# Kernel tuning notes

Hardware: AMD Instinct MI355X
Metric: run time of the kernel (lower is better)

The kernel has to match this reference:

```python
import jax, jax.numpy as jnp
import numpy as np

B, NM, MB, D = 16, 64, 64, 1024
NH, NKV, MEM = 16, 8, 64
HD = D // NH            # 64
S = MB + MEM            # per-step attention length
EPS = 1e-6

def precompute_freqs_cis(dim, end, theta=10000.0):
    freqs = 1.0 / (theta ** (jnp.arange(0, dim, 2)[: dim // 2].astype(jnp.float32) / dim))
    t = jnp.arange(end, dtype=jnp.float32)
    return jnp.exp(1j * jnp.outer(t, freqs))  # [end, dim//2] complex64

def apply_rope(x, fcis):
    # x: [s, h, d], fcis: [s, d//2] complex
    xc = x.reshape(x.shape[0], x.shape[1], HD // 2, 2)
    xc = jax.lax.complex(xc[..., 0], xc[..., 1]) * fcis[:, None, :]
    return jnp.stack([jnp.real(xc), jnp.imag(xc)], axis=-1).reshape(x.shape)

def layer_norm(x, scale, bias):
    m = x.mean(-1, keepdims=True)
    v = x.var(-1, keepdims=True)
    return (x - m) * jax.lax.rsqrt(v + EPS) * scale + bias

def setup_inputs() -> dict:
    key = jax.random.key(0)
    ks = jax.random.split(key, 8)
    s = 1.0 / np.sqrt(D)
    return {
        'hidden_states': jax.random.normal(ks[0], (B, NM, MB, D), jnp.float32),
        'mask': jax.random.bernoulli(ks[1], 0.9, (B, NM)),
        'mem_state': jax.random.normal(ks[2], (MEM, D), jnp.float32) * s,
        'wq': jax.random.normal(ks[3], (D, D), jnp.float32) * s,
        'wk': jax.random.normal(ks[4], (D, NKV * HD), jnp.float32) * s,
        'wv': jax.random.normal(ks[5], (D, NKV * HD), jnp.float32) * s,
        'wo': jax.random.normal(ks[6], (D, D), jnp.float32) * s,
        'pre_scale': jnp.ones((D,), jnp.float32),
        'pre_bias': jnp.zeros((D,), jnp.float32),
        'post_scale': jnp.ones((D,), jnp.float32),
        'post_bias': jnp.zeros((D,), jnp.float32),
    }

def reference(hidden_states, mask, mem_state, wq, wk, wv, wo, pre_scale, pre_bias, post_scale, post_bias):
    fcis = precompute_freqs_cis(HD, S)  # constant RoPE buffer, first S positions used
    rep = NH // NKV
    scale = 1.0 / np.sqrt(HD)

    def step(mem, inp):
        x_mb, m = inp  # x_mb: [MB, D], m: scalar bool
        h = layer_norm(jnp.concatenate([x_mb, mem], axis=0), pre_scale, pre_bias)  # [S, D]
        q = (h @ wq).reshape(S, NH, HD)
        k = (h @ wk).reshape(S, NKV, HD)
        v = (h @ wv).reshape(S, NKV, HD)
        q = apply_rope(q, fcis)
        k = apply_rope(k, fcis)
        k = jnp.repeat(k, rep, axis=1)  # GQA: expand kv heads
        v = jnp.repeat(v, rep, axis=1)
        qb, kb, vb = q.astype(jnp.bfloat16), k.astype(jnp.bfloat16), v.astype(jnp.bfloat16)
        logits = jnp.einsum('qhd,khd->hqk', qb, kb).astype(jnp.float32) * scale
        att = jax.nn.softmax(logits, axis=-1).astype(jnp.bfloat16)
        enc = jnp.einsum('hqk,khd->qhd', att, vb).reshape(S, D).astype(jnp.float32)
        out = enc[-MEM:] @ wo  # only memory-slot queries feed the update
        new_mem = layer_norm(out + mem, post_scale, post_bias)
        new_mem = jnp.where(m, new_mem, mem)  # lax.cond branch as select
        return new_mem, None

    def per_batch(x, m):
        final, _ = jax.lax.scan(step, mem_state, (x, m))
        return final

    return jax.vmap(per_batch)(hidden_states, mask)  # [B, MEM, D]
```

## Files before the change

kernel.cpp:

```cpp
#include <hip/hip_runtime.h>


typedef __attribute__((ext_vector_type(8))) _Float16 f16x8;
typedef __attribute__((ext_vector_type(4))) _Float16 f16x4;
typedef __attribute__((ext_vector_type(8))) short    s16x8;
typedef __attribute__((ext_vector_type(4))) float    f32x4;

#define NB   16
#define NMs  64
#define MBs  64
#define Dm   1024
#define NHh  16
#define NKVh 8
#define HDd  64
#define MEMm 64
#define Sq   128

__device__ __align__(16) _Float16      g_W1t[2048 * 1024];
__device__ __align__(16) _Float16      g_Wot[1024 * 1024];
__device__ __align__(16) float         g_rc[128 * 32];
__device__ __align__(16) float         g_rs[128 * 32];
__device__                unsigned char g_mask[NB * NMs];
__device__ __align__(16) _Float16      g_hx[(size_t)NB * NMs * MBs * Dm];
__device__ __align__(16) _Float16      g_hmem[NB * MEMm * Dm];
__device__ __align__(16) float         g_memA[NB * MEMm * Dm];
__device__ __align__(16) float         g_memB[NB * MEMm * Dm];
__device__ __align__(16) unsigned short g_qb[NB * NHh * 64 * 64];
__device__ __align__(16) unsigned short g_kb[NB * NKVh * 128 * 64];
__device__ __align__(16) unsigned short g_vt[NB * NKVh * 64 * 128];
__device__ __align__(16) _Float16      g_enc[NB * 64 * Dm];
__device__ __align__(16) float         g_outp[NB * 64 * Dm];

__device__ __forceinline__ unsigned short f2bf(float x) {
    union { float f; unsigned u; } v; v.f = x;
    unsigned u = v.u;
    return (unsigned short)((u + 0x7fffu + ((u >> 16) & 1u)) >> 16);
}
__device__ __forceinline__ float bf2f(unsigned short h) {
    union { unsigned u; float f; } v; v.u = ((unsigned)h) << 16; return v.f;
}

__device__ __forceinline__ void block_stats(float s, float ss, float eps,
                                            float* mean, float* rstd) {
    for (int off = 32; off > 0; off >>= 1) {
        s  += __shfl_down(s, off);
        ss += __shfl_down(ss, off);
    }
    __shared__ float red[8];
    int wid = threadIdx.x >> 6, lane = threadIdx.x & 63;
    __syncthreads();
    if (lane == 0) { red[wid] = s; red[4 + wid] = ss; }
    __syncthreads();
    float ts  = red[0] + red[1] + red[2] + red[3];
    float tss = red[4] + red[5] + red[6] + red[7];
    float m   = ts * (1.0f / 1024.0f);
    float var = tss * (1.0f / 1024.0f) - m * m;
    *mean = m;
    *rstd = rsqrtf(var + eps);
}

__global__ void k_transpose(const float* __restrict__ in, int ncols, int dsel) {
    _Float16* out = (dsel == 0) ? g_W1t
                  : (dsel == 1) ? (g_W1t + 1024 * 1024)
                  : (dsel == 2) ? (g_W1t + 1536 * 1024)
                                : g_Wot;
    __shared__ float tile[64][65];
    int bk = blockIdx.x, bn = blockIdx.y;
    int c = threadIdx.x & 63, rg = threadIdx.x >> 6;
    int k0 = bk * 64, n0 = bn * 64;
    for (int i = 0; i < 16; i++) {
        int r = rg * 16 + i;
        tile[r][c] = in[(size_t)(k0 + r) * ncols + n0 + c];
    }
    __syncthreads();
    for (int i = 0; i < 16; i++) {
        int r = rg * 16 + i;
        out[(size_t)(n0 + r) * 1024 + k0 + c] = (_Float16)tile[c][r];
    }
}

__global__ void k_rope() {
    int t = threadIdx.x;
    for (int j = 0; j < 32; j++) {
        double f = pow(10000.0, -(double)j / 32.0);
        double a = (double)t * f;
        g_rc[t * 32 + j] = (float)cos(a);
        g_rs[t * 32 + j] = (float)sin(a);
    }
}

__global__ void k_mask(const unsigned int* __restrict__ ip) {
    __shared__ int byteFmt;
    int t = threadIdx.x;
    if (t == 0) byteFmt = 0;
    __syncthreads();
    if (t < 256) {
        unsigned v = ip[t];
        if (!(v == 0u || v == 1u || v == 0x3F800000u)) byteFmt = 1;
    }
    __syncthreads();
    unsigned char m = byteFmt ? (((const unsigned char*)ip)[t] != 0)
                              : (ip[t] != 0u);
    g_mask[t] = m;
}

__global__ void k_ln_hx(const float* __restrict__ x,
                        const float* __restrict__ sc, const float* __restrict__ bi) {
    size_t row = blockIdx.x;
    int t = threadIdx.x;
    float4 v = ((const float4*)(x + row * 1024))[t];
    float mean, rstd;
    block_stats(v.x + v.y + v.z + v.w,
                v.x * v.x + v.y * v.y + v.z * v.z + v.w * v.w, 1e-6f, &mean, &rstd);
    float4 s4 = ((const float4*)sc)[t];
    float4 b4 = ((const float4*)bi)[t];
    f16x4 o;
    o[0] = (_Float16)((v.x - mean) * rstd * s4.x + b4.x);
    o[1] = (_Float16)((v.y - mean) * rstd * s4.y + b4.y);
    o[2] = (_Float16)((v.z - mean) * rstd * s4.z + b4.z);
    o[3] = (_Float16)((v.w - mean) * rstd * s4.w + b4.w);
    *(f16x4*)(g_hx + row * 1024 + t * 4) = o;
}

__global__ void k_ln_init(const float* __restrict__ ms,
                          const float* __restrict__ sc, const float* __restrict__ bi) {
    int b = blockIdx.x >> 6, r = blockIdx.x & 63;
    int t = threadIdx.x;
    float4 v = ((const float4*)(ms + (size_t)r * 1024))[t];
    ((float4*)(g_memA + ((size_t)b * 64 + r) * 1024))[t] = v;
    float mean, rstd;
    block_stats(v.x + v.y + v.z + v.w,
                v.x * v.x + v.y * v.y + v.z * v.z + v.w * v.w, 1e-6f, &mean, &rstd);
    float4 s4 = ((const float4*)sc)[t];
    float4 b4 = ((const float4*)bi)[t];
    f16x4 o;
    o[0] = (_Float16)((v.x - mean) * rstd * s4.x + b4.x);
    o[1] = (_Float16)((v.y - mean) * rstd * s4.y + b4.y);
    o[2] = (_Float16)((v.z - mean) * rstd * s4.z + b4.z);
    o[3] = (_Float16)((v.w - mean) * rstd * s4.w + b4.w);
    *(f16x4*)(g_hmem + ((size_t)b * 64 + r) * 1024 + t * 4) = o;
}

__device__ __forceinline__ void gemm_core(const _Float16* __restrict__ Abase,
                                          const _Float16* __restrict__ Bbase,
                                          _Float16* As, _Float16* Bs,
                                          f32x4 acc[2][2]) {
    int tid = threadIdx.x;
    int w = tid >> 6, l = tid & 63;
    int mo = (w & 1) * 32, no = (w >> 1) * 32;
    int sr = tid >> 2, sk = (tid & 3) * 8;
    int fr = l & 15, fq = (l >> 4) * 8;
    for (int kt = 0; kt < 32; ++kt) {
        f16x8 av = *(const f16x8*)(Abase + (size_t)sr * 1024 + kt * 32 + sk);
        f16x8 bv = *(const f16x8*)(Bbase + (size_t)sr * 1024 + kt * 32 + sk);
        __syncthreads();
        *(f16x8*)&As[sr * 40 + sk] = av;
        *(f16x8*)&Bs[sr * 40 + sk] = bv;
        __syncthreads();
        f16x8 a0 = *(const f16x8*)&As[(mo + fr) * 40 + fq];
        f16x8 a1 = *(const f16x8*)&As[(mo + 16 + fr) * 40 + fq];
        f16x8 b0 = *(const f16x8*)&Bs[(no + fr) * 40 + fq];
        f16x8 b1 = *(const f16x8*)&Bs[(no + 16 + fr) * 40 + fq];
        acc[0][0] = __builtin_amdgcn_mfma_f32_16x16x32_f16(a0, b0, acc[0][0], 0, 0, 0);
        acc[0][1] = __builtin_amdgcn_mfma_f32_16x16x32_f16(a0, b1, acc[0][1], 0, 0, 0);
        acc[1][0] = __builtin_amdgcn_mfma_f32_16x16x32_f16(a1, b0, acc[1][0], 0, 0, 0);
        acc[1][1] = __builtin_amdgcn_mfma_f32_16x16x32_f16(a1, b1, acc[1][1], 0, 0, 0);
    }
}

__launch_bounds__(256)
__global__ void k_gemm1(int s) {
    int bid = blockIdx.x;
    int b = bid / 48, t48 = bid % 48;
    int mtile = (t48 < 16) ? 0 : 1;
    int ntile = (t48 < 16) ? (16 + t48) : (t48 - 16);
    const _Float16* Abase = (mtile == 0)
        ? (g_hx + ((size_t)(b * NMs + s) * 64) * 1024)
        : (g_hmem + (size_t)b * 64 * 1024);
    const _Float16* Bbase = g_W1t + (size_t)ntile * 64 * 1024;
    __shared__ __align__(16) _Float16 As[64 * 40];
    __shared__ __align__(16) _Float16 Bs[64 * 40];
    f32x4 acc[2][2] = {};
    gemm_core(Abase, Bbase, As, Bs, acc);

    int tid = threadIdx.x, w = tid >> 6, l = tid & 63;
    int mo = (w & 1) * 32, no = (w >> 1) * 32;
    int quad = l >> 4, col = l & 15;
    int m0 = mtile * 64 + mo;
    int n0 = ntile * 64 + no;
    for (int i = 0; i < 2; i++)
        for (int j = 0; j < 2; j++)
            for (int r = 0; r < 4; r++) {
                float val = acc[i][j][r];
                float p = __shfl_xor(val, 1);
                int m = m0 + i * 16 + quad * 4 + r;
                int n = n0 + j * 16 + col;
                int d = n & 63;
                if (ntile < 16) {
                    int jj = d >> 1;
                    float c = g_rc[m * 32 + jj], sn = g_rs[m * 32 + jj];
                    float o = (d & 1) ? (p * sn + val * c) : (val * c - p * sn);
                    g_qb[(((size_t)b * 16 + ntile) * 64 + (m - 64)) * 64 + d] = f2bf(o);
                } else if (ntile < 24) {
                    int kvh = ntile - 16;
                    int jj = d >> 1;
                    float c = g_rc[m * 32 + jj], sn = g_rs[m * 32 + jj];
                    float o = (d & 1) ? (p * sn + val * c) : (val * c - p * sn);
                    g_kb[(((size_t)b * 8 + kvh) * 128 + m) * 64 + d] = f2bf(o);
                } else {
                    int kvh = ntile - 24;
                    g_vt[(((size_t)b * 8 + kvh) * 64 + d) * 128 + m] = f2bf(val);
                }
            }
}

__launch_bounds__(256)
__global__ void k_attn() {
    int b = blockIdx.x >> 4, h = blockIdx.x & 15, kvh = h >> 1;
    int tid = threadIdx.x, w = tid >> 6, l = tid & 63;
    int fr = l & 15, fq = (l >> 4) * 8;
    const unsigned short* qp = g_qb + ((size_t)b * 16 + h) * 64 * 64;
    const unsigned short* kp = g_kb + ((size_t)b * 8 + kvh) * 128 * 64;
    const unsigned short* vp = g_vt + ((size_t)b * 8 + kvh) * 64 * 128;

    s16x8 aq0 = *(const s16x8*)(qp + (w * 16 + fr) * 64 + fq);
    s16x8 aq1 = *(const s16x8*)(qp + (w * 16 + fr) * 64 + 32 + fq);
    f32x4 sc[8];
    for (int nt = 0; nt < 8; nt++) {
        sc[nt] = (f32x4){0.f, 0.f, 0.f, 0.f};
        s16x8 kb0 = *(const s16x8*)(kp + (nt * 16 + fr) * 64 + fq);
        s16x8 kb1 = *(const s16x8*)(kp + (nt * 16 + fr) * 64 + 32 + fq);
        sc[nt] = __builtin_amdgcn_mfma_f32_16x16x32_bf16(aq0, kb0, sc[nt], 0, 0, 0);
        sc[nt] = __builtin_amdgcn_mfma_f32_16x16x32_bf16(aq1, kb1, sc[nt], 0, 0, 0);
    }
    float lv[8][4];
    for (int nt = 0; nt < 8; nt++)
        for (int r = 0; r < 4; r++)
            lv[nt][r] = bf2f(f2bf(sc[nt][r])) * 0.125f;

    int quad = l >> 4;
    __shared__ __align__(16) unsigned short att_s[64 * 136];
    for (int r = 0; r < 4; r++) {
        float mx = -1e30f;
        for (int nt = 0; nt < 8; nt++) mx = fmaxf(mx, lv[nt][r]);
        for (int off = 1; off < 16; off <<= 1) mx = fmaxf(mx, __shfl_xor(mx, off));
        float sm = 0.f;
        for (int nt = 0; nt < 8; nt++) { lv[nt][r] = expf(lv[nt][r] - mx); sm += lv[nt][r]; }
        for (int off = 1; off < 16; off <<= 1) sm += __shfl_xor(sm, off);
        float inv = 1.0f / sm;
        int row = w * 16 + quad * 4 + r;
        for (int nt = 0; nt < 8; nt++)
            att_s[row * 136 + nt * 16 + fr] = f2bf(lv[nt][r] * inv);
    }
    f32x4 o[4];
    for (int nt = 0; nt < 4; nt++) o[nt] = (f32x4){0.f, 0.f, 0.f, 0.f};
    for (int kt = 0; kt < 4; kt++) {
        s16x8 a = *(const s16x8*)&att_s[(w * 16 + fr) * 136 + kt * 32 + fq];
        for (int nt = 0; nt < 4; nt++) {
            s16x8 bv = *(const s16x8*)(vp + (nt * 16 + fr) * 128 + kt * 32 + fq);
            o[nt] = __builtin_amdgcn_mfma_f32_16x16x32_bf16(a, bv, o[nt], 0, 0, 0);
        }
    }
    for (int nt = 0; nt < 4; nt++)
        for (int r = 0; r < 4; r++) {
            int m = w * 16 + quad * 4 + r;
            int d = nt * 16 + fr;
            g_enc[((size_t)b * 64 + m) * 1024 + h * 64 + d] =
                (_Float16)bf2f(f2bf(o[nt][r]));
        }
}

__launch_bounds__(256)
__global__ void k_gemm2() {
    int b = blockIdx.x >> 4, ntile = blockIdx.x & 15;
    const _Float16* Abase = g_enc + (size_t)b * 64 * 1024;
    const _Float16* Bbase = g_Wot + (size_t)ntile * 64 * 1024;
    __shared__ __align__(16) _Float16 As[64 * 40];
    __shared__ __align__(16) _Float16 Bs[64 * 40];
    f32x4 acc[2][2] = {};
    gemm_core(Abase, Bbase, As, Bs, acc);

    int tid = threadIdx.x, w = tid >> 6, l = tid & 63;
    int mo = (w & 1) * 32, no = (w >> 1) * 32;
    int quad = l >> 4, col = l & 15;
    for (int i = 0; i < 2; i++)
        for (int j = 0; j < 2; j++)
            for (int r = 0; r < 4; r++) {
                int m = mo + i * 16 + quad * 4 + r;
                int n = ntile * 64 + no + j * 16 + col;
                g_outp[((size_t)b * 64 + m) * 1024 + n] = acc[i][j][r];
            }
}

__global__ void k_ln2(int s, float* __restrict__ dout,
                      const float* __restrict__ psc, const float* __restrict__ pbi,
                      const float* __restrict__ qsc, const float* __restrict__ qbi) {
    int b = blockIdx.x >> 6, r = blockIdx.x & 63;
    const float* memIn = (s & 1) ? g_memB : g_memA;
    float* memOut = (s == 63) ? dout : ((s & 1) ? g_memA : g_memB);
    int t = threadIdx.x;
    size_t row = (size_t)b * 64 + r;
    float4 ov = ((const float4*)(g_outp + row * 1024))[t];
    float4 mv = ((const float4*)(memIn + row * 1024))[t];
    float4 y = {ov.x + mv.x, ov.y + mv.y, ov.z + mv.z, ov.w + mv.w};
    float mean, rstd;
    block_stats(y.x + y.y + y.z + y.w,
                y.x * y.x + y.y * y.y + y.z * y.z + y.w * y.w, 1e-6f, &mean, &rstd);
    float4 s4 = ((const float4*)psc)[t];
    float4 b4 = ((const float4*)pbi)[t];
    float4 nm = {(y.x - mean) * rstd * s4.x + b4.x,
                 (y.y - mean) * rstd * s4.y + b4.y,
                 (y.z - mean) * rstd * s4.z + b4.z,
                 (y.w - mean) * rstd * s4.w + b4.w};
    int mk = g_mask[b * 64 + s];
    float4 sel = mk ? nm : mv;
    ((float4*)(memOut + row * 1024))[t] = sel;
    float m2, rs2;
    block_stats(sel.x + sel.y + sel.z + sel.w,
                sel.x * sel.x + sel.y * sel.y + sel.z * sel.z + sel.w * sel.w,
                1e-6f, &m2, &rs2);
    float4 c4 = ((const float4*)qsc)[t];
    float4 d4 = ((const float4*)qbi)[t];
    f16x4 o;
    o[0] = (_Float16)((sel.x - m2) * rs2 * c4.x + d4.x);
    o[1] = (_Float16)((sel.y - m2) * rs2 * c4.y + d4.y);
    o[2] = (_Float16)((sel.z - m2) * rs2 * c4.z + d4.z);
    o[3] = (_Float16)((sel.w - m2) * rs2 * c4.w + d4.w);
    *(f16x4*)(g_hmem + row * 1024 + t * 4) = o;
}

extern "C" void kernel_launch(void* const* d_in, const int* in_sizes, int n_in,
                              void* d_out, int out_size, void* d_ws, size_t ws_size,
                              hipStream_t stream) {
    (void)in_sizes; (void)n_in; (void)d_ws; (void)ws_size; (void)out_size;
    const float* hidden    = (const float*)d_in[0];
    const unsigned int* mk = (const unsigned int*)d_in[1];
    const float* mem_state = (const float*)d_in[2];
    const float* wq  = (const float*)d_in[3];
    const float* wk  = (const float*)d_in[4];
    const float* wv  = (const float*)d_in[5];
    const float* wo  = (const float*)d_in[6];
    const float* pre_s  = (const float*)d_in[7];
    const float* pre_b  = (const float*)d_in[8];
    const float* post_s = (const float*)d_in[9];
    const float* post_b = (const float*)d_in[10];
    float* out = (float*)d_out;

    k_transpose<<<dim3(16, 16), 256, 0, stream>>>(wq, 1024, 0);
    k_transpose<<<dim3(16, 8),  256, 0, stream>>>(wk, 512, 1);
    k_transpose<<<dim3(16, 8),  256, 0, stream>>>(wv, 512, 2);
    k_transpose<<<dim3(16, 16), 256, 0, stream>>>(wo, 1024, 3);
    k_rope<<<1, 128, 0, stream>>>();
    k_mask<<<1, 1024, 0, stream>>>(mk);
    k_ln_hx<<<NB * NMs * MBs, 256, 0, stream>>>(hidden, pre_s, pre_b);
    k_ln_init<<<NB * MEMm, 256, 0, stream>>>(mem_state, pre_s, pre_b);

    for (int s = 0; s < NMs; ++s) {
        k_gemm1<<<NB * 48, 256, 0, stream>>>(s);
        k_attn<<<NB * NHh, 256, 0, stream>>>();
        k_gemm2<<<NB * 16, 256, 0, stream>>>();
        k_ln2<<<NB * MEMm, 256, 0, stream>>>(s, out, post_s, post_b, pre_s, pre_b);
    }
}
```

Measured before the change: 4.071 ms.

## Fuse per-step kernels via last-block atomic tickets and skip masked steps

Per-step launches drop from four to two. Attention is run by the last GEMM1 block to finish each head's Q/K/V tiles, tracked with atomic ticket counters. The post-LayerNorm and memory update run in the last GEMM2 block per batch. Steps whose mask is false return early, which is valid because the select keeps memory unchanged, and memory is updated in place instead of double-buffered. This cuts launch overhead and skips masked work, but the fused attention and LN tails run on only a few blocks, so parallelism is lower in those phases.

```diff
diff --git a/kernel.cpp b/kernel.cpp
--- a/kernel.cpp
+++ b/kernel.cpp
@@ -23,13 +23,14 @@
 __device__                unsigned char g_mask[NB * NMs];
 __device__ __align__(16) _Float16      g_hx[(size_t)NB * NMs * MBs * Dm];
 __device__ __align__(16) _Float16      g_hmem[NB * MEMm * Dm];
-__device__ __align__(16) float         g_memA[NB * MEMm * Dm];
-__device__ __align__(16) float         g_memB[NB * MEMm * Dm];
+__device__ __align__(16) float         g_mem[NB * MEMm * Dm];
 __device__ __align__(16) unsigned short g_qb[NB * NHh * 64 * 64];
 __device__ __align__(16) unsigned short g_kb[NB * NKVh * 128 * 64];
 __device__ __align__(16) unsigned short g_vt[NB * NKVh * 64 * 128];
 __device__ __align__(16) _Float16      g_enc[NB * 64 * Dm];
 __device__ __align__(16) float         g_outp[NB * 64 * Dm];
+__device__ unsigned int g_tk1[NB * NHh];
+__device__ unsigned int g_tk2[NB];
 
 __device__ __forceinline__ unsigned short f2bf(float x) {
     union { float f; unsigned u; } v; v.f = x;
@@ -127,7 +128,7 @@
     int b = blockIdx.x >> 6, r = blockIdx.x & 63;
     int t = threadIdx.x;
     float4 v = ((const float4*)(ms + (size_t)r * 1024))[t];
-    ((float4*)(g_memA + ((size_t)b * 64 + r) * 1024))[t] = v;
+    ((float4*)(g_mem + ((size_t)b * 64 + r) * 1024))[t] = v;
     float mean, rstd;
     block_stats(v.x + v.y + v.z + v.w,
                 v.x * v.x + v.y * v.y + v.z * v.z + v.w * v.w, 1e-6f, &mean, &rstd);
@@ -168,18 +169,74 @@
     }
 }
 
+__device__ void attn_one(int b, int h, unsigned short* att_s) {
+    int kvh = h >> 1;
+    int tid = threadIdx.x, w = tid >> 6, l = tid & 63;
+    int fr = l & 15, fq = (l >> 4) * 8;
+    const unsigned short* qp = g_qb + ((size_t)b * 16 + h) * 64 * 64;
+    const unsigned short* kp = g_kb + ((size_t)b * 8 + kvh) * 128 * 64;
+    const unsigned short* vp = g_vt + ((size_t)b * 8 + kvh) * 64 * 128;
+
+    s16x8 aq0 = *(const s16x8*)(qp + (w * 16 + fr) * 64 + fq);
+    s16x8 aq1 = *(const s16x8*)(qp + (w * 16 + fr) * 64 + 32 + fq);
+    f32x4 sc[8];
+    for (int nt = 0; nt < 8; nt++) {
+        sc[nt] = (f32x4){0.f, 0.f, 0.f, 0.f};
+        s16x8 kb0 = *(const s16x8*)(kp + (nt * 16 + fr) * 64 + fq);
+        s16x8 kb1 = *(const s16x8*)(kp + (nt * 16 + fr) * 64 + 32 + fq);
+        sc[nt] = __builtin_amdgcn_mfma_f32_16x16x32_bf16(aq0, kb0, sc[nt], 0, 0, 0);
+        sc[nt] = __builtin_amdgcn_mfma_f32_16x16x32_bf16(aq1, kb1, sc[nt], 0, 0, 0);
+    }
+    float lv[8][4];
+    for (int nt = 0; nt < 8; nt++)
+        for (int r = 0; r < 4; r++)
+            lv[nt][r] = bf2f(f2bf(sc[nt][r])) * 0.125f;
+
+    int quad = l >> 4;
+    for (int r = 0; r < 4; r++) {
+        float mx = -1e30f;
+        for (int nt = 0; nt < 8; nt++) mx = fmaxf(mx, lv[nt][r]);
+        for (int off = 1; off < 16; off <<= 1) mx = fmaxf(mx, __shfl_xor(mx, off));
+        float sm = 0.f;
+        for (int nt = 0; nt < 8; nt++) { lv[nt][r] = expf(lv[nt][r] - mx); sm += lv[nt][r]; }
+        for (int off = 1; off < 16; off <<= 1) sm += __shfl_xor(sm, off);
+        float inv = 1.0f / sm;
+        int row = w * 16 + quad * 4 + r;
+        for (int nt = 0; nt < 8; nt++)
+            att_s[row * 136 + nt * 16 + fr] = f2bf(lv[nt][r] * inv);
+    }
+    f32x4 o[4];
+    for (int nt = 0; nt < 4; nt++) o[nt] = (f32x4){0.f, 0.f, 0.f, 0.f};
+    for (int kt = 0; kt < 4; kt++) {
+        s16x8 a = *(const s16x8*)&att_s[(w * 16 + fr) * 136 + kt * 32 + fq];
+        for (int nt = 0; nt < 4; nt++) {
+            s16x8 bv = *(const s16x8*)(vp + (nt * 16 + fr) * 128 + kt * 32 + fq);
+            o[nt] = __builtin_amdgcn_mfma_f32_16x16x32_bf16(a, bv, o[nt], 0, 0, 0);
+        }
+    }
+    for (int nt = 0; nt < 4; nt++)
+        for (int r = 0; r < 4; r++) {
+            int m = w * 16 + quad * 4 + r;
+            int d = nt * 16 + fr;
+            g_enc[((size_t)b * 64 + m) * 1024 + h * 64 + d] =
+                (_Float16)bf2f(f2bf(o[nt][r]));
+        }
+}
+
 __launch_bounds__(256)
-__global__ void k_gemm1(int s) {
+__global__ void k_step1(int s) {
     int bid = blockIdx.x;
     int b = bid / 48, t48 = bid % 48;
+    if (!g_mask[b * 64 + s]) return;
     int mtile = (t48 < 16) ? 0 : 1;
     int ntile = (t48 < 16) ? (16 + t48) : (t48 - 16);
     const _Float16* Abase = (mtile == 0)
         ? (g_hx + ((size_t)(b * NMs + s) * 64) * 1024)
         : (g_hmem + (size_t)b * 64 * 1024);
     const _Float16* Bbase = g_W1t + (size_t)ntile * 64 * 1024;
-    __shared__ __align__(16) _Float16 As[64 * 40];
-    __shared__ __align__(16) _Float16 Bs[64 * 40];
+    __shared__ __align__(16) unsigned char smem[64 * 136 * 2];
+    _Float16* As = (_Float16*)smem;
+    _Float16* Bs = (_Float16*)(smem + 64 * 40 * 2);
     f32x4 acc[2][2] = {};
     gemm_core(Abase, Bbase, As, Bs, acc);
 
@@ -212,67 +269,103 @@
                     g_vt[(((size_t)b * 8 + kvh) * 64 + d) * 128 + m] = f2bf(val);
                 }
             }
+
+    int kvh = (ntile < 16) ? (ntile >> 1) : ((ntile < 24) ? (ntile - 16) : (ntile - 24));
+    __threadfence();
+    __shared__ int s_wm;
+    if (tid == 0) {
+        int wm = 0;
+        if (ntile < 16) {
+            if (atomicAdd(&g_tk1[b * 16 + ntile], 1u) == 4u) wm = 1 << (ntile & 1);
+        } else {
+            if (atomicAdd(&g_tk1[b * 16 + 2 * kvh], 1u) == 4u)     wm |= 1;
+            if (atomicAdd(&g_tk1[b * 16 + 2 * kvh + 1], 1u) == 4u) wm |= 2;
+        }
+        s_wm = wm;
+    }
+    __syncthreads();
+    int wm = s_wm;
+    if (!wm) return;
+    __threadfence();
+    unsigned short* att_s = (unsigned short*)smem;
+    if (wm & 1) attn_one(b, 2 * kvh,     att_s);
+    if (wm & 2) attn_one(b, 2 * kvh + 1, att_s);
+    if (tid == 0) {
+        if (wm & 1) atomicExch(&g_tk1[b * 16 + 2 * kvh],     0u);
+        if (wm & 2) atomicExch(&g_tk1[b * 16 + 2 * kvh + 1], 0u);
+    }
+}
+
+__device__ void ln_tail(int b, int s, float* __restrict__ dout,
+                        const float* __restrict__ psc, const float* __restrict__ pbi,
+                        const float* __restrict__ qsc, const float* __restrict__ qbi) {
+    int tid = threadIdx.x, w = tid >> 6, l = tid & 63;
+    float psA[16], pbA[16], qsA[16], qbA[16];
+#pragma unroll
+    for (int j = 0; j < 4; j++) {
+        float4 t;
+        t = ((const float4*)psc)[l * 4 + j]; psA[j*4]=t.x; psA[j*4+1]=t.y; psA[j*4+2]=t.z; psA[j*4+3]=t.w;
+        t = ((const float4*)pbi)[l * 4 + j]; pbA[j*4]=t.x; pbA[j*4+1]=t.y; pbA[j*4+2]=t.z; pbA[j*4+3]=t.w;
+        t = ((const float4*)qsc)[l * 4 + j]; qsA[j*4]=t.x; qsA[j*4+1]=t.y; qsA[j*4+2]=t.z; qsA[j*4+3]=t.w;
+        t = ((const float4*)qbi)[l * 4 + j]; qbA[j*4]=t.x; qbA[j*4+1]=t.y; qbA[j*4+2]=t.z; qbA[j*4+3]=t.w;
+    }
+    for (int r = w; r < 64; r += 4) {
+        size_t row = (size_t)b * 64 + r;
+        const float4* op = (const float4*)(g_outp + row * 1024) + l * 4;
+        float4*       mp = (float4*)(g_mem + row * 1024) + l * 4;
+        float y[16];
+        float sm = 0.f, ss = 0.f;
+#pragma unroll
+        for (int j = 0; j < 4; j++) {
+            float4 o = op[j], m = mp[j];
+            y[j*4+0] = o.x + m.x; y[j*4+1] = o.y + m.y;
+            y[j*4+2] = o.z + m.z; y[j*4+3] = o.w + m.w;
+        }
+#pragma unroll
+        for (int i = 0; i < 16; i++) { sm += y[i]; ss += y[i] * y[i]; }
+        for (int off = 32; off > 0; off >>= 1) { sm += __shfl_xor(sm, off); ss += __shfl_xor(ss, off); }
+        float mean = sm * (1.0f / 1024.0f);
+        float rstd = rsqrtf(ss * (1.0f / 1024.0f) - mean * mean + 1e-6f);
+        float nm[16];
+#pragma unroll
+        for (int i = 0; i < 16; i++) nm[i] = (y[i] - mean) * rstd * psA[i] + pbA[i];
+#pragma unroll
+        for (int j = 0; j < 4; j++) {
+            float4 v4 = {nm[j*4+0], nm[j*4+1], nm[j*4+2], nm[j*4+3]};
+            mp[j] = v4;
+            if (s == NMs - 1) ((float4*)(dout + row * 1024))[l * 4 + j] = v4;
+        }
+        float s2 = 0.f, s2s = 0.f;
+#pragma unroll
+        for (int i = 0; i < 16; i++) { s2 += nm[i]; s2s += nm[i] * nm[i]; }
+        for (int off = 32; off > 0; off >>= 1) { s2 += __shfl_xor(s2, off); s2s += __shfl_xor(s2s, off); }
+        float mean2 = s2 * (1.0f / 1024.0f);
+        float rstd2 = rsqrtf(s2s * (1.0f / 1024.0f) - mean2 * mean2 + 1e-6f);
+        f16x8 h0, h1;
+#pragma unroll
+        for (int i = 0; i < 8; i++) h0[i] = (_Float16)((nm[i]     - mean2) * rstd2 * qsA[i]     + qbA[i]);
+#pragma unroll
+        for (int i = 0; i < 8; i++) h1[i] = (_Float16)((nm[8 + i] - mean2) * rstd2 * qsA[8 + i] + qbA[8 + i]);
+        *(f16x8*)(g_hmem + row * 1024 + l * 16)     = h0;
+        *(f16x8*)(g_hmem + row * 1024 + l * 16 + 8) = h1;
+    }
 }
 
 __launch_bounds__(256)
-__global__ void k_attn() {
-    int b = blockIdx.x >> 4, h = blockIdx.x & 15, kvh = h >> 1;
-    int tid = threadIdx.x, w = tid >> 6, l = tid & 63;
-    int fr = l & 15, fq = (l >> 4) * 8;
-    const unsigned short* qp = g_qb + ((size_t)b * 16 + h) * 64 * 64;
-    const unsigned short* kp = g_kb + ((size_t)b * 8 + kvh) * 128 * 64;
-    const unsigned short* vp = g_vt + ((size_t)b * 8 + kvh) * 64 * 128;
-
-    s16x8 aq0 = *(const s16x8*)(qp + (w * 16 + fr) * 64 + fq);
-    s16x8 aq1 = *(const s16x8*)(qp + (w * 16 + fr) * 64 + 32 + fq);
-    f32x4 sc[8];
-    for (int nt = 0; nt < 8; nt++) {
-        sc[nt] = (f32x4){0.f, 0.f, 0.f, 0.f};
-        s16x8 kb0 = *(const s16x8*)(kp + (nt * 16 + fr) * 64 + fq);
-        s16x8 kb1 = *(const s16x8*)(kp + (nt * 16 + fr) * 64 + 32 + fq);
-        sc[nt] = __builtin_amdgcn_mfma_f32_16x16x32_bf16(aq0, kb0, sc[nt], 0, 0, 0);
-        sc[nt] = __builtin_amdgcn_mfma_f32_16x16x32_bf16(aq1, kb1, sc[nt], 0, 0, 0);
-    }
-    float lv[8][4];
-    for (int nt = 0; nt < 8; nt++)
-        for (int r = 0; r < 4; r++)
-            lv[nt][r] = bf2f(f2bf(sc[nt][r])) * 0.125f;
-
-    int quad = l >> 4;
-    __shared__ __align__(16) unsigned short att_s[64 * 136];
-    for (int r = 0; r < 4; r++) {
-        float mx = -1e30f;
-        for (int nt = 0; nt < 8; nt++) mx = fmaxf(mx, lv[nt][r]);
-        for (int off = 1; off < 16; off <<= 1) mx = fmaxf(mx, __shfl_xor(mx, off));
-        float sm = 0.f;
-        for (int nt = 0; nt < 8; nt++) { lv[nt][r] = expf(lv[nt][r] - mx); sm += lv[nt][r]; }
-        for (int off = 1; off < 16; off <<= 1) sm += __shfl_xor(sm, off);
-        float inv = 1.0f / sm;
-        int row = w * 16 + quad * 4 + r;
-        for (int nt = 0; nt < 8; nt++)
-            att_s[row * 136 + nt * 16 + fr] = f2bf(lv[nt][r] * inv);
-    }
-    f32x4 o[4];
-    for (int nt = 0; nt < 4; nt++) o[nt] = (f32x4){0.f, 0.f, 0.f, 0.f};
-    for (int kt = 0; kt < 4; kt++) {
-        s16x8 a = *(const s16x8*)&att_s[(w * 16 + fr) * 136 + kt * 32 + fq];
-        for (int nt = 0; nt < 4; nt++) {
-            s16x8 bv = *(const s16x8*)(vp + (nt * 16 + fr) * 128 + kt * 32 + fq);
-            o[nt] = __builtin_amdgcn_mfma_f32_16x16x32_bf16(a, bv, o[nt], 0, 0, 0);
-        }
-    }
-    for (int nt = 0; nt < 4; nt++)
-        for (int r = 0; r < 4; r++) {
-            int m = w * 16 + quad * 4 + r;
-            int d = nt * 16 + fr;
-            g_enc[((size_t)b * 64 + m) * 1024 + h * 64 + d] =
-                (_Float16)bf2f(f2bf(o[nt][r]));
-        }
-}
-
-__launch_bounds__(256)
-__global__ void k_gemm2() {
+__global__ void k_step2(int s, float* __restrict__ dout,
+                        const float* __restrict__ psc, const float* __restrict__ pbi,
+                        const float* __restrict__ qsc, const float* __restrict__ qbi) {
     int b = blockIdx.x >> 4, ntile = blockIdx.x & 15;
+    int tid = threadIdx.x;
+    if (!g_mask[b * 64 + s]) {
+        if (s == NMs - 1) {
+            int r = ntile * 4 + (tid >> 6), l = tid & 63;
+            const float4* src = (const float4*)(g_mem + ((size_t)b * 64 + r) * 1024);
+            float4*       dst = (float4*)(dout + ((size_t)b * 64 + r) * 1024);
+            for (int j = 0; j < 4; j++) dst[l * 4 + j] = src[l * 4 + j];
+        }
+        return;
+    }
     const _Float16* Abase = g_enc + (size_t)b * 64 * 1024;
     const _Float16* Bbase = g_Wot + (size_t)ntile * 64 * 1024;
     __shared__ __align__(16) _Float16 As[64 * 40];
@@ -280,7 +373,7 @@
     f32x4 acc[2][2] = {};
     gemm_core(Abase, Bbase, As, Bs, acc);
 
-    int tid = threadIdx.x, w = tid >> 6, l = tid & 63;
+    int w = tid >> 6, l = tid & 63;
     int mo = (w & 1) * 32, no = (w >> 1) * 32;
     int quad = l >> 4, col = l & 15;
     for (int i = 0; i < 2; i++)
@@ -290,43 +383,15 @@
                 int n = ntile * 64 + no + j * 16 + col;
                 g_outp[((size_t)b * 64 + m) * 1024 + n] = acc[i][j][r];
             }
-}
-
-__global__ void k_ln2(int s, float* __restrict__ dout,
-                      const float* __restrict__ psc, const float* __restrict__ pbi,
-                      const float* __restrict__ qsc, const float* __restrict__ qbi) {
-    int b = blockIdx.x >> 6, r = blockIdx.x & 63;
-    const float* memIn = (s & 1) ? g_memB : g_memA;
-    float* memOut = (s == 63) ? dout : ((s & 1) ? g_memA : g_memB);
-    int t = threadIdx.x;
-    size_t row = (size_t)b * 64 + r;
-    float4 ov = ((const float4*)(g_outp + row * 1024))[t];
-    float4 mv = ((const float4*)(memIn + row * 1024))[t];
-    float4 y = {ov.x + mv.x, ov.y + mv.y, ov.z + mv.z, ov.w + mv.w};
-    float mean, rstd;
-    block_stats(y.x + y.y + y.z + y.w,
-                y.x * y.x + y.y * y.y + y.z * y.z + y.w * y.w, 1e-6f, &mean, &rstd);
-    float4 s4 = ((const float4*)psc)[t];
-    float4 b4 = ((const float4*)pbi)[t];
-    float4 nm = {(y.x - mean) * rstd * s4.x + b4.x,
-                 (y.y - mean) * rstd * s4.y + b4.y,
-                 (y.z - mean) * rstd * s4.z + b4.z,
-                 (y.w - mean) * rstd * s4.w + b4.w};
-    int mk = g_mask[b * 64 + s];
-    float4 sel = mk ? nm : mv;
-    ((float4*)(memOut + row * 1024))[t] = sel;
-    float m2, rs2;
-    block_stats(sel.x + sel.y + sel.z + sel.w,
-                sel.x * sel.x + sel.y * sel.y + sel.z * sel.z + sel.w * sel.w,
-                1e-6f, &m2, &rs2);
-    float4 c4 = ((const float4*)qsc)[t];
-    float4 d4 = ((const float4*)qbi)[t];
-    f16x4 o;
-    o[0] = (_Float16)((sel.x - m2) * rs2 * c4.x + d4.x);
-    o[1] = (_Float16)((sel.y - m2) * rs2 * c4.y + d4.y);
-    o[2] = (_Float16)((sel.z - m2) * rs2 * c4.z + d4.z);
-    o[3] = (_Float16)((sel.w - m2) * rs2 * c4.w + d4.w);
-    *(f16x4*)(g_hmem + row * 1024 + t * 4) = o;
+
+    __threadfence();
+    __shared__ int s_win;
+    if (tid == 0) s_win = (atomicAdd(&g_tk2[b], 1u) == 15u);
+    __syncthreads();
+    if (!s_win) return;
+    __threadfence();
+    ln_tail(b, s, dout, psc, pbi, qsc, qbi);
+    if (tid == 0) atomicExch(&g_tk2[b], 0u);
 }
 
 extern "C" void kernel_launch(void* const* d_in, const int* in_sizes, int n_in,
@@ -356,9 +421,7 @@
     k_ln_init<<<NB * MEMm, 256, 0, stream>>>(mem_state, pre_s, pre_b);
 
     for (int s = 0; s < NMs; ++s) {
-        k_gemm1<<<NB * 48, 256, 0, stream>>>(s);
-        k_attn<<<NB * NHh, 256, 0, stream>>>();
-        k_gemm2<<<NB * 16, 256, 0, stream>>>();
-        k_ln2<<<NB * MEMm, 256, 0, stream>>>(s, out, post_s, post_b, pre_s, pre_b);
-    }
-}
+        k_step1<<<NB * 48, 256, 0, stream>>>(s);
+        k_step2<<<NB * 16, 256, 0, stream>>>(s, out, post_s, post_b, pre_s, pre_b);
+    }
+}
```

After: 15.28 ms. 3.75x slower.
